# Optimization experiments

Measured on AMD Instinct MI355X. Metric: run time of the kernel, lower is better.

The kernel has to match this reference:

```python
import jax, jax.numpy as jnp
import numpy as np
from jax.scipy.special import logsumexp

SIZE = 68          # DP length (self.size)
SSN = 8            # number of secondary-structure classes
C = SSN + 1        # states per step
S1 = SIZE + 1      # positions
BATCH = 256


def setup_inputs() -> dict:
    key = jax.random.key(0)
    k1, k2, k3, k4 = jax.random.split(key, 4)
    P = jax.random.normal(k1, (BATCH, 1, C, S1, S1), jnp.float32)
    Q = jax.random.normal(k2, (1, C, C, S1, S1), jnp.float32)
    pi = jax.random.normal(k3, (C,), jnp.float32)
    T = jnp.ones((1,), jnp.float32)
    ls = jax.random.randint(k4, (BATCH,), 0, S1, dtype=jnp.int32)
    return {"P": P, "Q": Q, "pi": pi, "T": T, "ls": ls}


def _max_alpha(P, Q, pi, T):
    # Viterbi-style max-plus recursion with logsumexp renormalization.
    b = P.shape[0]
    a0 = jnp.full((b, C, S1), -jnp.inf, P.dtype).at[:, :, 0].set(pi[None, :])
    n0 = logsumexp(a0, axis=(-1, -2), keepdims=True)      # (b,1,1)
    a0 = a0 - n0

    def step(carry, _):
        la, ln = carry                                    # (b,C,S1), (b,1,1)
        # broadcast sum over (b, c_prev, c_new, t_prev, t_new)
        M = P + T * Q + la[:, :, None, :, None]
        a = M.max(axis=(1, 3))                            # max over c_prev, t_prev -> (b,C,S1)
        n = ln + logsumexp(a, axis=(-1, -2), keepdims=True)
        a = a + ln - n
        return (a, n), (a, n)

    _, (a_seq, n_seq) = jax.lax.scan(step, (a0, n0), None, length=SIZE)
    a_all = jnp.concatenate([a0[None], a_seq], 0)          # (S1, b, C, S1) forward order
    n_all = jnp.concatenate([n0[None], n_seq], 0)          # (S1, b, 1, 1)
    # torch code stacks alpha REVERSED but norm in forward order, then adds
    alpha = a_all[::-1] + n_all
    return jnp.swapaxes(alpha, 0, 1)                       # (b, SIZE+1, C, S1)


def _backtrace(alpha, P, Q, T, ls):
    b = alpha.shape[0]
    Ps = P[:, 0]            # (b, C, S1, S1)
    Qs = Q[0]               # (C, C, S1, S1)
    bi = jnp.arange(b)
    c0 = jnp.full((b,), 3, jnp.int32)
    l0 = jnp.zeros((b,), jnp.int32)
    t0 = ls.astype(jnp.int32)

    def step(carry, a):
        c, l, t = carry
        Pterm = Ps[bi, c, :, t]                 # (b, S1)
        Qterm = Qs[c, :, :, t]                  # (b, C, S1)
        score = Pterm[:, None, :] + T * Qterm + a
        idx = jnp.argmax(score.reshape(b, -1), axis=-1).astype(jnp.int32)
        cn = idx // S1
        tn = idx % S1
        ln = tn - t
        return (cn, ln, tn), (cn, ln, tn)

    a_seq = jnp.swapaxes(alpha, 0, 1)[1:]       # (SIZE, b, C, S1)
    _, (cs, lss, ts) = jax.lax.scan(step, (c0, l0, t0), a_seq)
    c_all = jnp.concatenate([c0[None], cs], 0)[::-1]   # (SIZE+1, b)
    l_all = jnp.concatenate([l0[None], lss], 0)[::-1]
    t_all = jnp.concatenate([t0[None], ts], 0)[::-1]
    mp = jnp.swapaxes(jnp.stack([c_all, l_all, t_all], -1), 0, 1)  # (b, SIZE+1, 3)
    # shift length column: mp[:, :-1, 1] = mp[:, 1:, 1]; mp[:, -1, 1] = 0
    l_shift = jnp.concatenate([mp[:, 1:, 1], jnp.zeros((b, 1), jnp.int32)], 1)
    return mp.at[:, :, 1].set(l_shift)


def reference(P, Q, pi, T, ls):
    alpha = _max_alpha(P, Q, pi, T)
    max_pattern = _backtrace(alpha, P, Q, T, ls)
    return alpha, max_pattern
```

## Files before the change

kernel.cpp:

```cpp
#include <hip/hip_runtime.h>

#define C9     9
#define S1     69
#define JT     621
#define NBATCH 256
#define NSTEP  68
#define QJ     4761
#define QI     42849
#define BROW   42849
#define ALPHA_N (NBATCH*BROW)
#define QTFL   385664
#define NEGINF (-__builtin_inff())

typedef float float4u __attribute__((ext_vector_type(4), aligned(4)));

__global__ void qw_kernel(const float* __restrict__ Q, float* __restrict__ QW)
{
  const int bl = blockIdx.x;
  const int j = bl / S1, s = bl - j*S1;
  float* dst = QW + (size_t)bl*JT;
  const float* src = Q + (size_t)j*QJ + s*S1;
  for (int f = threadIdx.x; f < JT; f += 256){
    const int i = f / S1, t = f - i*S1;
    dst[f] = src[i*QJ + t];
  }
}

__global__ void qtrans_kernel(const float* __restrict__ Q, float* __restrict__ QT)
{
  __shared__ float tile[69*70];
  const int pl = blockIdx.x;
  const int c = pl / 9, i = pl - c*9;
  const float* src = Q + (size_t)pl*QJ;
  for (int f = threadIdx.x; f < QJ; f += 256){
    const int s = f / S1, t = f - s*S1;
    tile[s*70 + t] = src[f];
  }
  __syncthreads();
  float* dst = QT + (size_t)c*QI + i*S1;
  for (int f = threadIdx.x; f < QJ; f += 256){
    const int t = f / S1, s = f - t*S1;
    dst[t*JT + s] = tile[s*70 + t];
  }
}

template<int SI, int SS>
__device__ __forceinline__ float4u scan12(const float* __restrict__ qb,
                                          const float* __restrict__ pb,
                                          const float* __restrict__ laS,
                                          const float Tv)
{
#define LD(BUF, PV, S) { \
  const float* q_ = qb + (S)*SS; \
  _Pragma("unroll") \
  for (int i_ = 0; i_ < C9; ++i_) BUF[i_] = *(const float4u*)(q_ + i_*SI); \
  PV = *(const float4u*)(pb + (S)*S1); }
#define CM(BUF, PV, S) { \
  float r0=NEGINF, r1=NEGINF, r2=NEGINF, r3=NEGINF; \
  _Pragma("unroll") \
  for (int i_ = 0; i_ < C9; ++i_){ \
    const float lv_ = laS[i_*72 + (S)]; \
    r0 = fmaxf(r0, fmaf(Tv, BUF[i_].x, lv_)); \
    r1 = fmaxf(r1, fmaf(Tv, BUF[i_].y, lv_)); \
    r2 = fmaxf(r2, fmaf(Tv, BUF[i_].z, lv_)); \
    r3 = fmaxf(r3, fmaf(Tv, BUF[i_].w, lv_)); \
  } \
  acc.x = fmaxf(acc.x, PV.x + r0); acc.y = fmaxf(acc.y, PV.y + r1); \
  acc.z = fmaxf(acc.z, PV.z + r2); acc.w = fmaxf(acc.w, PV.w + r3); }

  float4u acc; acc.x = acc.y = acc.z = acc.w = NEGINF;
  float4u qA[C9], qB[C9], pA, pB;
  int s = 0;
  LD(qA, pA, s)
  for (; s + 2 < 12; s += 2){
    LD(qB, pB, s+1)
    CM(qA, pA, s)
    LD(qA, pA, s+2)
    CM(qB, pB, s+1)
  }
  LD(qB, pB, s+1)
  CM(qA, pA, s)
  CM(qB, pB, s+1)
  return acc;
#undef LD
#undef CM
}

__global__ __launch_bounds__(1024) void mega_kernel(
    const float* __restrict__ P, const float* __restrict__ Q,
    const float* __restrict__ pi, const float* __restrict__ Tp,
    const int* __restrict__ ls, float* __restrict__ out,
    const float* __restrict__ QW, const float* __restrict__ QT, int wsmode)
{
  __shared__ __align__(16) float la[2][C9*72];
  __shared__ float part[5][162][4];
  __shared__ float red[16];
  __shared__ float m_sh[NSTEP+1], lse_sh[NSTEP+1], n_sh[NSTEP+1];
  __shared__ float sums_sh[NSTEP+1][3];
  __shared__ float sbest[16];
  __shared__ int   sidx[16];
  __shared__ int   sct[2];

  const int tid  = threadIdx.x;
  const int w    = tid >> 6;
  const int lane = tid & 63;
  const int b    = blockIdx.x;
  const bool act = tid < 972;
  const int gg   = act ? tid / 162 : 5;
  const int slot = act ? tid - gg*162 : 0;
  const int j    = slot / 18;
  const int tq   = slot - j*18;
  const int t0   = (tq < 17) ? 4*tq : 65;
  const int s_lo = (gg*23) >> 1;
  const float Tv = Tp[0];

  float* outb = out + (size_t)b*BROW;

  for (int e = tid; e < JT; e += 1024){
    const int i = e / S1, s = e - i*S1;
    const float v0 = (s == 0) ? pi[i] : NEGINF;
    outb[68*JT + e] = v0;
    la[0][i*72 + s] = v0;
  }
  if (tid == 0){
    float mx = pi[0];
    #pragma unroll
    for (int c = 1; c < C9; ++c) mx = fmaxf(mx, pi[c]);
    float sm = 0.f;
    #pragma unroll
    for (int c = 0; c < C9; ++c) sm += expf(pi[c] - mx);
    m_sh[0]   = mx;
    lse_sh[0] = mx + logf(sm);
  }
  __syncthreads();
  float mprev = m_sh[0];

  const bool useQW = (wsmode >= 1);
  const float* qw_b = QW + (size_t)j*QI + (size_t)s_lo*JT + t0;
  const float* qr_b = Q + (size_t)j*QJ + s_lo*S1 + t0;
  const float* p_b  = P + (size_t)(b*C9 + j)*QJ + s_lo*S1 + t0;

  int cur = 0;
  for (int k = 1; k <= NSTEP; ++k){
    const float* laS = la[cur] + s_lo;
    float4u acc;
    if (act){
      if (useQW) acc = scan12<S1, JT>(qw_b, p_b, laS, Tv);
      else       acc = scan12<QI, S1>(qr_b, p_b, laS, Tv);
      if (gg > 0){
        part[gg-1][slot][0] = acc.x; part[gg-1][slot][1] = acc.y;
        part[gg-1][slot][2] = acc.z; part[gg-1][slot][3] = acc.w;
      }
    }
    __syncthreads();

    float mval = NEGINF;
    float v0 = 0.f, v1 = 0.f, v2 = 0.f, v3 = 0.f;
    if (act && gg == 0){
      float c0 = acc.x, c1 = acc.y, c2 = acc.z, c3 = acc.w;
      #pragma unroll
      for (int g = 0; g < 5; ++g){
        c0 = fmaxf(c0, part[g][slot][0]);
        c1 = fmaxf(c1, part[g][slot][1]);
        c2 = fmaxf(c2, part[g][slot][2]);
        c3 = fmaxf(c3, part[g][slot][3]);
      }
      v0 = c0 - mprev; v1 = c1 - mprev; v2 = c2 - mprev; v3 = c3 - mprev;
      float* dst = outb + (size_t)(68-k)*JT + j*S1 + t0;
      if (tq < 17){
        float4u vv; vv.x = v0; vv.y = v1; vv.z = v2; vv.w = v3;
        *(float4u*)dst = vv;
        *(float4*)(&la[cur^1][j*72 + t0]) = make_float4(v0, v1, v2, v3);
        mval = fmaxf(fmaxf(v0, v1), fmaxf(v2, v3));
      } else {
        dst[3] = v3;
        la[cur^1][j*72 + 68] = v3;
        mval = v3;
      }
    }
    float mr = mval;
    #pragma unroll
    for (int o = 32; o >= 1; o >>= 1) mr = fmaxf(mr, __shfl_down(mr, o));
    if (lane == 0) red[w] = mr;
    __syncthreads();
    const float mA = fmaxf(fmaxf(red[0], red[1]), red[2]);
    if (act && gg == 0){
      float sv = (tq < 17)
        ? expf(v0 - mA) + expf(v1 - mA) + expf(v2 - mA) + expf(v3 - mA)
        : expf(v3 - mA);
      #pragma unroll
      for (int o = 32; o >= 1; o >>= 1) sv += __shfl_down(sv, o);
      if (lane == 0) sums_sh[k][w] = sv;
    }
    if (tid == 0) m_sh[k] = mA;
    mprev = mA;
    cur ^= 1;
  }
  __syncthreads();

  if (tid == 0){
    double dd = 0.0;
    for (int kk = 0; kk <= NSTEP; ++kk){
      float lse;
      if (kk == 0) lse = lse_sh[0];
      else lse = m_sh[kk] + logf(sums_sh[kk][0] + sums_sh[kk][1] + sums_sh[kk][2]);
      lse_sh[kk] = lse;
      n_sh[kk] = (float)((double)lse + dd);
      dd += (double)m_sh[kk];
    }
  }
  __syncthreads();

  for (int K = 0; K <= NSTEP; ++K){
    const float Cst = n_sh[K] - lse_sh[68-K];
    for (int e = tid; e < JT; e += 1024){
      float* r = outb + (size_t)K*JT + e;
      *r = fmaxf(*r + Cst, -3.0e38f);
    }
  }
  __syncthreads();

  {
    int c = 3, t2 = ls[b];
    float* mpb = out + (size_t)ALPHA_N + (size_t)b*(69*3);
    if (tid == 0){
      mpb[68*3+0] = 3.f; mpb[68*3+1] = 0.f; mpb[68*3+2] = (float)t2;
      mpb[67*3+1] = 0.f;
    }
    const bool vok = tid < JT;
    const int etid = vok ? tid : 0;
    const int im = etid / S1;
    const int sm = etid - im*S1;
    float av = vok ? outb[1*JT + tid] : NEGINF;
    for (int r = 1; r <= NSTEP; ++r){
      float avn = NEGINF;
      if (r < NSTEP && vok) avn = outb[(size_t)(r+1)*JT + tid];
      float best = NEGINF; int bidx = 0x7fffffff;
      if (vok){
        float qv;
        if (wsmode >= 2)      qv = QT[(size_t)c*QI + (size_t)t2*JT + tid];
        else if (wsmode == 1) qv = QW[(size_t)c*QI + (size_t)sm*JT + im*S1 + t2];
        else                  qv = Q[(size_t)c*QI + (size_t)im*QJ + sm*S1 + t2];
        const float pv = P[(size_t)(b*C9 + c)*QJ + sm*S1 + t2];
        best = (pv + Tv*qv) + av;
        bidx = tid;
      }
      #pragma unroll
      for (int o = 32; o >= 1; o >>= 1){
        const float ov = __shfl_down(best, o); const int oi = __shfl_down(bidx, o);
        if (ov > best || (ov == best && oi < bidx)){ best = ov; bidx = oi; }
      }
      if (lane == 0){ sbest[w] = best; sidx[w] = bidx; }
      __syncthreads();
      if (tid == 0){
        float bb = sbest[0]; int bi = sidx[0];
        #pragma unroll
        for (int q = 1; q < 16; ++q)
          if (sbest[q] > bb || (sbest[q] == bb && sidx[q] < bi)){
            bb = sbest[q]; bi = sidx[q];
          }
        const int cn = bi / S1, tn = bi - cn*S1;
        mpb[(68-r)*3 + 0] = (float)cn;
        mpb[(68-r)*3 + 2] = (float)tn;
        if (r <= 67) mpb[(67-r)*3 + 1] = (float)(tn - t2);
        sct[0] = cn; sct[1] = tn;
      }
      __syncthreads();
      c = sct[0]; t2 = sct[1];
      av = avn;
    }
  }
}

extern "C" void kernel_launch(void* const* d_in, const int* in_sizes, int n_in,
                              void* d_out, int out_size, void* d_ws, size_t ws_size,
                              hipStream_t stream)
{
  const float* P  = (const float*)d_in[0];
  const float* Q  = (const float*)d_in[1];
  const float* pi = (const float*)d_in[2];
  const float* T  = (const float*)d_in[3];
  const int*   ls = (const int*)d_in[4];

  float* out = (float*)d_out;

  int wsmode = 0; float* QW = nullptr; float* QT = nullptr;
  if (ws_size >= (size_t)QTFL*4){ wsmode = 1; QW = (float*)d_ws; }
  if (ws_size >= (size_t)2*QTFL*4){ wsmode = 2; QT = (float*)d_ws + QTFL; }

  if (wsmode >= 1) qw_kernel<<<JT, 256, 0, stream>>>(Q, QW);
  if (wsmode >= 2) qtrans_kernel<<<81, 256, 0, stream>>>(Q, QT);
  mega_kernel<<<NBATCH, 1024, 0, stream>>>(P, Q, pi, T, ls, out, QW, QT, wsmode);
}
```

Baseline: 2.218 ms.

## Repartition DP step work into three source groups of two outputs each

Each step's thread-to-work mapping changes from six source-position groups, each thread owning four outputs over 12 source positions, to three groups, each thread owning two outputs over 23 source positions. This cuts the cross-group partial-max reduction through shared memory from five partials to two and shrinks register buffers. In exchange, Q and P loads drop from 16-byte to 8-byte vectors, and the P load is no longer prefetched ahead of compute. The reduction bookkeeping (red and sums arrays) grows from three to five wavefronts.

```diff
diff --git a/kernel.cpp b/kernel.cpp
--- a/kernel.cpp
+++ b/kernel.cpp
@@ -12,7 +12,7 @@
 #define QTFL   385664
 #define NEGINF (-__builtin_inff())
 
-typedef float float4u __attribute__((ext_vector_type(4), aligned(4)));
+typedef float float2u __attribute__((ext_vector_type(2), aligned(4)));
 
 __global__ void qw_kernel(const float* __restrict__ Q, float* __restrict__ QW)
 {
@@ -45,42 +45,38 @@
 }
 
 template<int SI, int SS>
-__device__ __forceinline__ float4u scan12(const float* __restrict__ qb,
+__device__ __forceinline__ float2u scan23(const float* __restrict__ qb,
                                           const float* __restrict__ pb,
                                           const float* __restrict__ laS,
                                           const float Tv)
 {
-#define LD(BUF, PV, S) { \
+#define LD(QB, S) { \
   const float* q_ = qb + (S)*SS; \
   _Pragma("unroll") \
-  for (int i_ = 0; i_ < C9; ++i_) BUF[i_] = *(const float4u*)(q_ + i_*SI); \
-  PV = *(const float4u*)(pb + (S)*S1); }
-#define CM(BUF, PV, S) { \
-  float r0=NEGINF, r1=NEGINF, r2=NEGINF, r3=NEGINF; \
+  for (int i_ = 0; i_ < C9; ++i_) QB[i_] = *(const float2u*)(q_ + i_*SI); }
+#define CM(QB, S) { \
+  const float2u pv_ = *(const float2u*)(pb + (S)*S1); \
+  float r0 = NEGINF, r1 = NEGINF; \
   _Pragma("unroll") \
   for (int i_ = 0; i_ < C9; ++i_){ \
     const float lv_ = laS[i_*72 + (S)]; \
-    r0 = fmaxf(r0, fmaf(Tv, BUF[i_].x, lv_)); \
-    r1 = fmaxf(r1, fmaf(Tv, BUF[i_].y, lv_)); \
-    r2 = fmaxf(r2, fmaf(Tv, BUF[i_].z, lv_)); \
-    r3 = fmaxf(r3, fmaf(Tv, BUF[i_].w, lv_)); \
+    r0 = fmaxf(r0, fmaf(Tv, QB[i_].x, lv_)); \
+    r1 = fmaxf(r1, fmaf(Tv, QB[i_].y, lv_)); \
   } \
-  acc.x = fmaxf(acc.x, PV.x + r0); acc.y = fmaxf(acc.y, PV.y + r1); \
-  acc.z = fmaxf(acc.z, PV.z + r2); acc.w = fmaxf(acc.w, PV.w + r3); }
-
-  float4u acc; acc.x = acc.y = acc.z = acc.w = NEGINF;
-  float4u qA[C9], qB[C9], pA, pB;
+  acc.x = fmaxf(acc.x, pv_.x + r0); \
+  acc.y = fmaxf(acc.y, pv_.y + r1); }
+
+  float2u acc; acc.x = acc.y = NEGINF;
+  float2u qA[C9], qB[C9];
+  LD(qA, 0)
   int s = 0;
-  LD(qA, pA, s)
-  for (; s + 2 < 12; s += 2){
-    LD(qB, pB, s+1)
-    CM(qA, pA, s)
-    LD(qA, pA, s+2)
-    CM(qB, pB, s+1)
-  }
-  LD(qB, pB, s+1)
-  CM(qA, pA, s)
-  CM(qB, pB, s+1)
+  for (; s + 2 < 23; s += 2){
+    LD(qB, s+1)
+    CM(qA, s)
+    LD(qA, s+2)
+    CM(qB, s+1)
+  }
+  CM(qA, 22)
   return acc;
 #undef LD
 #undef CM
@@ -93,10 +89,10 @@
     const float* __restrict__ QW, const float* __restrict__ QT, int wsmode)
 {
   __shared__ __align__(16) float la[2][C9*72];
-  __shared__ float part[5][162][4];
+  __shared__ float part[2][315][3];
   __shared__ float red[16];
   __shared__ float m_sh[NSTEP+1], lse_sh[NSTEP+1], n_sh[NSTEP+1];
-  __shared__ float sums_sh[NSTEP+1][3];
+  __shared__ float sums_sh[NSTEP+1][5];
   __shared__ float sbest[16];
   __shared__ int   sidx[16];
   __shared__ int   sct[2];
@@ -105,13 +101,14 @@
   const int w    = tid >> 6;
   const int lane = tid & 63;
   const int b    = blockIdx.x;
-  const bool act = tid < 972;
-  const int gg   = act ? tid / 162 : 5;
-  const int slot = act ? tid - gg*162 : 0;
-  const int j    = slot / 18;
-  const int tq   = slot - j*18;
-  const int t0   = (tq < 17) ? 4*tq : 65;
-  const int s_lo = (gg*23) >> 1;
+  const bool act = tid < 945;
+  const int gg   = act ? tid / 315 : 2;
+  const int slot = act ? tid - gg*315 : 314;
+  const int j    = slot / 35;
+  const int tp   = slot - j*35;
+  const bool own2 = (tp < 34);
+  const int t0   = own2 ? 2*tp : 67;
+  const int s_lo = gg*23;
   const float Tv = Tp[0];
 
   float* outb = out + (size_t)b*BROW;
@@ -143,39 +140,35 @@
   int cur = 0;
   for (int k = 1; k <= NSTEP; ++k){
     const float* laS = la[cur] + s_lo;
-    float4u acc;
+    float2u acc;
     if (act){
-      if (useQW) acc = scan12<S1, JT>(qw_b, p_b, laS, Tv);
-      else       acc = scan12<QI, S1>(qr_b, p_b, laS, Tv);
+      if (useQW) acc = scan23<S1, JT>(qw_b, p_b, laS, Tv);
+      else       acc = scan23<QI, S1>(qr_b, p_b, laS, Tv);
       if (gg > 0){
-        part[gg-1][slot][0] = acc.x; part[gg-1][slot][1] = acc.y;
-        part[gg-1][slot][2] = acc.z; part[gg-1][slot][3] = acc.w;
+        part[gg-1][slot][0] = acc.x;
+        part[gg-1][slot][1] = acc.y;
       }
     }
     __syncthreads();
 
     float mval = NEGINF;
-    float v0 = 0.f, v1 = 0.f, v2 = 0.f, v3 = 0.f;
+    float v0 = 0.f, v1 = 0.f;
     if (act && gg == 0){
-      float c0 = acc.x, c1 = acc.y, c2 = acc.z, c3 = acc.w;
-      #pragma unroll
-      for (int g = 0; g < 5; ++g){
-        c0 = fmaxf(c0, part[g][slot][0]);
-        c1 = fmaxf(c1, part[g][slot][1]);
-        c2 = fmaxf(c2, part[g][slot][2]);
-        c3 = fmaxf(c3, part[g][slot][3]);
-      }
-      v0 = c0 - mprev; v1 = c1 - mprev; v2 = c2 - mprev; v3 = c3 - mprev;
+      const float c0 = fmaxf(fmaxf(acc.x, part[0][slot][0]), part[1][slot][0]);
+      const float c1 = fmaxf(fmaxf(acc.y, part[0][slot][1]), part[1][slot][1]);
+      v0 = c0 - mprev;
+      v1 = c1 - mprev;
       float* dst = outb + (size_t)(68-k)*JT + j*S1 + t0;
-      if (tq < 17){
-        float4u vv; vv.x = v0; vv.y = v1; vv.z = v2; vv.w = v3;
-        *(float4u*)dst = vv;
-        *(float4*)(&la[cur^1][j*72 + t0]) = make_float4(v0, v1, v2, v3);
-        mval = fmaxf(fmaxf(v0, v1), fmaxf(v2, v3));
+      if (own2){
+        float2u vv; vv.x = v0; vv.y = v1;
+        *(float2u*)dst = vv;
+        la[cur^1][j*72 + t0]     = v0;
+        la[cur^1][j*72 + t0 + 1] = v1;
+        mval = fmaxf(v0, v1);
       } else {
-        dst[3] = v3;
-        la[cur^1][j*72 + 68] = v3;
-        mval = v3;
+        dst[1] = v1;
+        la[cur^1][j*72 + 68] = v1;
+        mval = v1;
       }
     }
     float mr = mval;
@@ -183,11 +176,11 @@
     for (int o = 32; o >= 1; o >>= 1) mr = fmaxf(mr, __shfl_down(mr, o));
     if (lane == 0) red[w] = mr;
     __syncthreads();
-    const float mA = fmaxf(fmaxf(red[0], red[1]), red[2]);
+    float mA = red[0];
+    #pragma unroll
+    for (int q = 1; q < 5; ++q) mA = fmaxf(mA, red[q]);
     if (act && gg == 0){
-      float sv = (tq < 17)
-        ? expf(v0 - mA) + expf(v1 - mA) + expf(v2 - mA) + expf(v3 - mA)
-        : expf(v3 - mA);
+      float sv = own2 ? (expf(v0 - mA) + expf(v1 - mA)) : expf(v1 - mA);
       #pragma unroll
       for (int o = 32; o >= 1; o >>= 1) sv += __shfl_down(sv, o);
       if (lane == 0) sums_sh[k][w] = sv;
@@ -203,7 +196,12 @@
     for (int kk = 0; kk <= NSTEP; ++kk){
       float lse;
       if (kk == 0) lse = lse_sh[0];
-      else lse = m_sh[kk] + logf(sums_sh[kk][0] + sums_sh[kk][1] + sums_sh[kk][2]);
+      else {
+        float S = sums_sh[kk][0];
+        #pragma unroll
+        for (int q = 1; q < 5; ++q) S += sums_sh[kk][q];
+        lse = m_sh[kk] + logf(S);
+      }
       lse_sh[kk] = lse;
       n_sh[kk] = (float)((double)lse + dd);
       dd += (double)m_sh[kk];
```

New measurement: 2.058 ms. 1.08x faster.
